# Optimization experiments

Measured on AMD Instinct MI355X. Metric: run time of the kernel, lower is better.

## Reference

```python
import jax, jax.numpy as jnp
import numpy as np

BATCH = 512
FEATURES = 256
BITS = 8
ENC = FEATURES * BITS          # 2048
HIDDEN = 8192
CLASSES = 1000
K_SYN = 32                     # synapses per segment
THRESH = 16                    # segmentActivationThreshold
VMIN, VMAX = 0.0, 1.0


def _make_synapse_matrix(key, num_neurons, prev_size, k):
    """Dense (num_neurons, prev_size) matrix with k random +/-1 synapses per neuron."""
    kc, ks = jax.random.split(key)
    cols = jax.random.randint(kc, (num_neurons, k), 0, prev_size)
    signs = jnp.where(jax.random.bernoulli(ks, 0.5, (num_neurons, k)), 1.0, -1.0)
    rows = jnp.broadcast_to(jnp.arange(num_neurons)[:, None], (num_neurons, k))
    W = jnp.zeros((num_neurons, prev_size), dtype=jnp.float32)
    return W.at[rows, cols].set(signs.astype(jnp.float32))


def gray_code_encode(x, num_bits, vmin, vmax):
    # (batch, features) -> (batch, features*bits) binary float
    levels = jnp.round(
        jnp.clip(x, vmin, vmax) / (vmax - vmin) * (2 ** num_bits - 1)
    ).astype(jnp.int32)
    gray = levels ^ (levels >> 1)
    bits = (gray[..., None] >> jnp.arange(num_bits)) & 1  # (b, f, bits)
    return bits.astype(jnp.float32).reshape(x.shape[0], -1)


def setup_inputs() -> dict:
    key = jax.random.key(0)
    kx, k1, k2, ko = jax.random.split(key, 4)
    x = jax.random.uniform(kx, (BATCH, FEATURES), dtype=jnp.float32)
    W1 = _make_synapse_matrix(k1, HIDDEN, ENC, K_SYN)
    W2 = _make_synapse_matrix(k2, HIDDEN, HIDDEN, K_SYN)
    # Output connections: float (useBinaryOutputConnections=False); small random
    # stand-in for trained connection strengths.
    Wout = jax.random.normal(ko, (2, HIDDEN, CLASSES), dtype=jnp.float32) * 0.02
    return {"x": x, "W1": W1, "W2": W2, "Wout": Wout}


def reference(x, W1, W2, Wout):
    # Encode continuous input to binary gray-code activations.
    a0 = gray_code_encode(x, BITS, VMIN, VMAX)          # (B, ENC)
    # Hidden layer 1: binary synapse matmul + threshold activation.
    z1 = a0 @ W1.T                                      # (B, HIDDEN)
    a1 = (z1 >= THRESH).astype(jnp.float32)
    # Hidden layer 2.
    z2 = a1 @ W2.T                                      # (B, HIDDEN)
    a2 = (z2 >= THRESH).astype(jnp.float32)
    # Output accumulation across all hidden layers.
    out = a1 @ Wout[0] + a2 @ Wout[1]                   # (B, CLASSES)
    predictions = jnp.argmax(out, axis=-1)
    return predictions, out
```

## Files before the change

kernel.cpp:

```cpp
#include <hip/hip_runtime.h>

#define BATCH 512
#define FEATURES 256
#define ENC 2048
#define HIDDEN 8192
#define CLASSES 1000
#define THRESH 16
#define MAXACT 256
#define NPREP 16
#define PAIR_CAP 65536

typedef unsigned long long u64;
typedef unsigned int u32;

#define OFF_A0T    0
#define OFF_NPAIRS 131072
#define OFF_PAIRS  131136


__global__ __launch_bounds__(256) void prep_kernel(const float* __restrict__ x,
                                                   u32* __restrict__ a0t_w,
                                                   u32* __restrict__ npairs) {
    int bid = blockIdx.x;
    int tid = threadIdx.x;
    if (bid == 0 && tid == 0) npairs[0] = 0;

    __shared__ float xs[32][256];
    for (int r = 0; r < 32; ++r)
        xs[r][tid] = x[(size_t)(bid * 32 + r) * FEATURES + tid];
    __syncthreads();

    u32 m[8] = {0,0,0,0,0,0,0,0};
    for (int i = 0; i < 32; ++i) {
        float v = xs[i][tid];
        v = fminf(fmaxf(v, 0.0f), 1.0f);
        int lvl = (int)rintf(v * 255.0f);
        int g = lvl ^ (lvl >> 1);
        u32 bit = 1u << i;
#pragma unroll
        for (int k = 0; k < 8; ++k) if ((g >> k) & 1) m[k] |= bit;
    }
#pragma unroll
    for (int k = 0; k < 8; ++k) a0t_w[(tid * 8 + k) * 16 + bid] = m[k];
}

__global__ __launch_bounds__(256) void z1_kernel(const float* __restrict__ W1,
                                                 const unsigned char* __restrict__ a0t,
                                                 u32* __restrict__ pairs,
                                                 u32* __restrict__ npairs) {
    int wid = threadIdx.x >> 6, lane = threadIdx.x & 63;
    int n = blockIdx.x * 4 + wid;
    const float4* rowv = reinterpret_cast<const float4*>(W1 + (size_t)n * ENC);
    __shared__ int colsAll[4][40];
    int* cols = colsAll[wid];

    float4 v[8];
#pragma unroll
    for (int it = 0; it < 8; ++it) v[it] = rowv[it * 64 + lane];

    int cnt = 0;
    u64 lmask = (lane == 63) ? 0x7fffffffffffffffULL : ((1ULL << lane) - 1ULL);
#pragma unroll
    for (int it = 0; it < 8; ++it) {
#pragma unroll
        for (int c = 0; c < 4; ++c) {
            float vc = (c == 0) ? v[it].x : (c == 1) ? v[it].y
                     : (c == 2) ? v[it].z : v[it].w;
            u64 mm = __ballot(vc != 0.0f);
            if (vc != 0.0f) {
                int pos = cnt + __popcll(mm & lmask);
                cols[pos] = ((it * 256 + lane * 4 + c) << 1) | (vc < 0.0f ? 1 : 0);
            }
            cnt += __popcll(mm);
        }
    }

    u32 p0=0,p1=0,p2=0,p3=0,p4=0,p5=0;
    u32 q0=0,q1=0,q2=0,q3=0,q4=0,q5=0;
#pragma unroll 8
    for (int i = 0; i < cnt; ++i) {
        int e = __builtin_amdgcn_readfirstlane(cols[i]);
        u32 m = a0t[(size_t)(e >> 1) * 64 + lane];
        if (e & 1) {
            u32 t;
            t = q0 & m; q0 ^= m; m = t;
            t = q1 & m; q1 ^= m; m = t;
            t = q2 & m; q2 ^= m; m = t;
            t = q3 & m; q3 ^= m; m = t;
            t = q4 & m; q4 ^= m; m = t;
            q5 ^= m;
        } else {
            u32 t;
            t = p0 & m; p0 ^= m; m = t;
            t = p1 & m; p1 ^= m; m = t;
            t = p2 & m; p2 ^= m; m = t;
            t = p3 & m; p3 ^= m; m = t;
            p5 ^= (p4 & m); p4 ^= m;
        }
    }

    u32 cand = p4 | p5;
    while (cand) {
        int k = __ffs(cand) - 1;
        cand &= cand - 1;
        int P = ((p0 >> k) & 1) | (((p1 >> k) & 1) << 1) | (((p2 >> k) & 1) << 2) |
                (((p3 >> k) & 1) << 3) | (((p4 >> k) & 1) << 4) | (((p5 >> k) & 1) << 5);
        int N = ((q0 >> k) & 1) | (((q1 >> k) & 1) << 1) | (((q2 >> k) & 1) << 2) |
                (((q3 >> k) & 1) << 3) | (((q4 >> k) & 1) << 4) | (((q5 >> k) & 1) << 5);
        if (P - N >= THRESH) {
            int b = lane * 8 + k;
            u32 pos = atomicAdd(npairs, 1u);
            if (pos < PAIR_CAP) pairs[pos] = ((u32)b << 13) | (u32)n;
        }
    }
}

__global__ __launch_bounds__(256) void out_kernel(const float* __restrict__ W2,
                                                  const float* __restrict__ Wout,
                                                  const u32* __restrict__ pairs,
                                                  const u32* __restrict__ npairs,
                                                  float* __restrict__ outp,
                                                  float* __restrict__ pred) {
    int b = blockIdx.x;
    int tid = threadIdx.x;
    __shared__ int act1[MAXACT], act2[MAXACT];
    __shared__ int n1s, n2s;
    __shared__ float rv[256];
    __shared__ int ri[256];

    if (tid == 0) { n1s = 0; n2s = 0; }
    __syncthreads();

    int tot = (int)npairs[0];
    if (tot > PAIR_CAP) tot = PAIR_CAP;
    for (int i = tid; i < tot; i += 256) {
        u32 p = pairs[i];
        if ((int)(p >> 13) == b) {
            int pos = atomicAdd(&n1s, 1);
            if (pos < MAXACT) act1[pos] = (int)(p & 8191u);
        }
    }
    __syncthreads();
    if (tid == 0) {
        int c = n1s; if (c > MAXACT) { c = MAXACT; n1s = c; }
        for (int i = 1; i < c; ++i) {
            int vv = act1[i], k = i;
            while (k > 0 && act1[k - 1] > vv) { act1[k] = act1[k - 1]; --k; }
            act1[k] = vv;
        }
    }
    __syncthreads();
    int na1 = n1s;

    if (na1 >= THRESH) {
        for (int nn = tid; nn < HIDDEN; nn += 256) {
            int z = 0;
            for (int i = 0; i < na1; ++i) z += (int)W2[(size_t)nn * HIDDEN + act1[i]];
            if (z >= THRESH) {
                int pos = atomicAdd(&n2s, 1);
                if (pos < MAXACT) act2[pos] = nn;
            }
        }
        __syncthreads();
        if (tid == 0) {
            int c = n2s; if (c > MAXACT) { c = MAXACT; n2s = c; }
            for (int i = 1; i < c; ++i) {
                int vv = act2[i], k = i;
                while (k > 0 && act2[k - 1] > vv) { act2[k] = act2[k - 1]; --k; }
                act2[k] = vv;
            }
        }
        __syncthreads();
    }
    int na2 = n2s;

    float s0 = 0.f, s1 = 0.f, s2 = 0.f, s3 = 0.f;
    for (int i = 0; i < na1; ++i) {
        const float* wr = Wout + (size_t)act1[i] * CLASSES;
        s0 += wr[tid]; s1 += wr[tid + 256]; s2 += wr[tid + 512];
        if (tid + 768 < CLASSES) s3 += wr[tid + 768];
    }
    for (int i = 0; i < na2; ++i) {
        const float* wr = Wout + (size_t)HIDDEN * CLASSES + (size_t)act2[i] * CLASSES;
        s0 += wr[tid]; s1 += wr[tid + 256]; s2 += wr[tid + 512];
        if (tid + 768 < CLASSES) s3 += wr[tid + 768];
    }

    float* orow = outp + (size_t)b * CLASSES;
    orow[tid] = s0; orow[tid + 256] = s1; orow[tid + 512] = s2;
    if (tid + 768 < CLASSES) orow[tid + 768] = s3;

    float best = s0; int bi = tid;
    if (s1 > best) { best = s1; bi = tid + 256; }
    if (s2 > best) { best = s2; bi = tid + 512; }
    if (tid + 768 < CLASSES && s3 > best) { best = s3; bi = tid + 768; }
    rv[tid] = best; ri[tid] = bi;
    __syncthreads();
    for (int off = 128; off; off >>= 1) {
        if (tid < off) {
            float ov = rv[tid + off]; int oi = ri[tid + off];
            if (ov > rv[tid] || (ov == rv[tid] && oi < ri[tid])) { rv[tid] = ov; ri[tid] = oi; }
        }
        __syncthreads();
    }
    if (tid == 0) pred[b] = (float)ri[0];
}

extern "C" void kernel_launch(void* const* d_in, const int* in_sizes, int n_in,
                              void* d_out, int out_size, void* d_ws, size_t ws_size,
                              hipStream_t stream) {
    (void)in_sizes; (void)n_in; (void)out_size; (void)ws_size;
    const float* x    = (const float*)d_in[0];
    const float* W1   = (const float*)d_in[1];
    const float* W2   = (const float*)d_in[2];
    const float* Wout = (const float*)d_in[3];

    float* pred = (float*)d_out;
    float* outp = (float*)d_out + BATCH;

    char* ws = (char*)d_ws;
    u32* a0t_w  = (u32*)(ws + OFF_A0T);
    u32* npairs = (u32*)(ws + OFF_NPAIRS);
    u32* pairs  = (u32*)(ws + OFF_PAIRS);

    prep_kernel<<<NPREP, 256, 0, stream>>>(x, a0t_w, npairs);
    z1_kernel<<<HIDDEN / 4, 256, 0, stream>>>(W1, (const unsigned char*)a0t_w,
                                              pairs, npairs);
    out_kernel<<<BATCH, 256, 0, stream>>>(W2, Wout, pairs, npairs, outp, pred);
}
```

Measured before the change: 38.20 us.

## Fuse gray-code prep into z1 kernel with per-block LDS bitmaps and slot output

Result: slower. 88.78 us (+132.4%).

```diff
diff --git a/kernel.cpp b/kernel.cpp
--- a/kernel.cpp
+++ b/kernel.cpp
@@ -7,118 +7,148 @@
 #define CLASSES 1000
 #define THRESH 16
 #define MAXACT 256
-#define NPREP 16
-#define PAIR_CAP 65536
+#define NBLK1 256
+#define THR1 1024
+#define ROWS_PER_BLK 32
+#define SLOTS 64
 
 typedef unsigned long long u64;
 typedef unsigned int u32;
 
-#define OFF_A0T    0
-#define OFF_NPAIRS 131072
-#define OFF_PAIRS  131136
-
-
-__global__ __launch_bounds__(256) void prep_kernel(const float* __restrict__ x,
-                                                   u32* __restrict__ a0t_w,
-                                                   u32* __restrict__ npairs) {
+#define OFF_CNTS  0
+#define OFF_PAIRS 1024
+
+__global__ __launch_bounds__(THR1, 4) void z1_fused(
+    const float* __restrict__ x, const float* __restrict__ W1,
+    u32* __restrict__ cnts, u32* __restrict__ pairs)
+{
+    __shared__ u32 a0t[ENC * 16];
+    __shared__ int colsAll[16][2][40];
+    __shared__ int lcnt;
+
+    int tid = threadIdx.x;
+    int wv = tid >> 6, lane = tid & 63;
     int bid = blockIdx.x;
-    int tid = threadIdx.x;
-    if (bid == 0 && tid == 0) npairs[0] = 0;
-
-    __shared__ float xs[32][256];
-    for (int r = 0; r < 32; ++r)
-        xs[r][tid] = x[(size_t)(bid * 32 + r) * FEATURES + tid];
-    __syncthreads();
-
-    u32 m[8] = {0,0,0,0,0,0,0,0};
-    for (int i = 0; i < 32; ++i) {
-        float v = xs[i][tid];
-        v = fminf(fmaxf(v, 0.0f), 1.0f);
-        int lvl = (int)rintf(v * 255.0f);
-        int g = lvl ^ (lvl >> 1);
-        u32 bit = 1u << i;
-#pragma unroll
-        for (int k = 0; k < 8; ++k) if ((g >> k) & 1) m[k] |= bit;
-    }
-#pragma unroll
-    for (int k = 0; k < 8; ++k) a0t_w[(tid * 8 + k) * 16 + bid] = m[k];
-}
-
-__global__ __launch_bounds__(256) void z1_kernel(const float* __restrict__ W1,
-                                                 const unsigned char* __restrict__ a0t,
-                                                 u32* __restrict__ pairs,
-                                                 u32* __restrict__ npairs) {
-    int wid = threadIdx.x >> 6, lane = threadIdx.x & 63;
-    int n = blockIdx.x * 4 + wid;
-    const float4* rowv = reinterpret_cast<const float4*>(W1 + (size_t)n * ENC);
-    __shared__ int colsAll[4][40];
-    int* cols = colsAll[wid];
-
-    float4 v[8];
-#pragma unroll
-    for (int it = 0; it < 8; ++it) v[it] = rowv[it * 64 + lane];
-
-    int cnt = 0;
+    if (tid == 0) lcnt = 0;
+
+    int n0 = bid * ROWS_PER_BLK + wv * 2;
+    const float4* r0 = reinterpret_cast<const float4*>(W1 + (size_t)n0 * ENC);
+    const float4* r1 = reinterpret_cast<const float4*>(W1 + (size_t)(n0 + 1) * ENC);
+    float4 va[8], vb[8];
+#pragma unroll
+    for (int it = 0; it < 8; ++it) va[it] = r0[it * 64 + lane];
+#pragma unroll
+    for (int it = 0; it < 8; ++it) vb[it] = r1[it * 64 + lane];
+
+    {
+        int w = tid & 15;
+        int fbase = tid >> 4;
+#pragma unroll
+        for (int j = 0; j < 4; ++j) {
+            int f = fbase + 64 * j;
+            u32 m[8] = {0, 0, 0, 0, 0, 0, 0, 0};
+#pragma unroll 4
+            for (int i = 0; i < 32; ++i) {
+                float v = x[(size_t)(w * 32 + i) * FEATURES + f];
+                v = fminf(fmaxf(v, 0.0f), 1.0f);
+                int lvl = (int)rintf(v * 255.0f);
+                int g = lvl ^ (lvl >> 1);
+#pragma unroll
+                for (int k = 0; k < 8; ++k)
+                    m[k] |= (u32)((g >> k) & 1) << i;
+            }
+#pragma unroll
+            for (int k = 0; k < 8; ++k)
+                a0t[(f * 8 + k) * 16 + w] = m[k];
+        }
+    }
+
     u64 lmask = (lane == 63) ? 0x7fffffffffffffffULL : ((1ULL << lane) - 1ULL);
+    int ca = 0, cb = 0;
 #pragma unroll
     for (int it = 0; it < 8; ++it) {
 #pragma unroll
         for (int c = 0; c < 4; ++c) {
-            float vc = (c == 0) ? v[it].x : (c == 1) ? v[it].y
-                     : (c == 2) ? v[it].z : v[it].w;
+            float vc = (c == 0) ? va[it].x : (c == 1) ? va[it].y
+                     : (c == 2) ? va[it].z : va[it].w;
             u64 mm = __ballot(vc != 0.0f);
             if (vc != 0.0f) {
-                int pos = cnt + __popcll(mm & lmask);
-                cols[pos] = ((it * 256 + lane * 4 + c) << 1) | (vc < 0.0f ? 1 : 0);
-            }
-            cnt += __popcll(mm);
-        }
-    }
-
-    u32 p0=0,p1=0,p2=0,p3=0,p4=0,p5=0;
-    u32 q0=0,q1=0,q2=0,q3=0,q4=0,q5=0;
+                int pos = ca + __popcll(mm & lmask);
+                colsAll[wv][0][pos] = ((it * 256 + lane * 4 + c) << 1) | (vc < 0.0f ? 1 : 0);
+            }
+            ca += __popcll(mm);
+        }
+    }
+#pragma unroll
+    for (int it = 0; it < 8; ++it) {
+#pragma unroll
+        for (int c = 0; c < 4; ++c) {
+            float vc = (c == 0) ? vb[it].x : (c == 1) ? vb[it].y
+                     : (c == 2) ? vb[it].z : vb[it].w;
+            u64 mm = __ballot(vc != 0.0f);
+            if (vc != 0.0f) {
+                int pos = cb + __popcll(mm & lmask);
+                colsAll[wv][1][pos] = ((it * 256 + lane * 4 + c) << 1) | (vc < 0.0f ? 1 : 0);
+            }
+            cb += __popcll(mm);
+        }
+    }
+
+    __syncthreads();
+
+    const unsigned char* a0b = (const unsigned char*)a0t;
+    for (int rr = 0; rr < 2; ++rr) {
+        int cnt = (rr == 0) ? ca : cb;
+        int n = n0 + rr;
+        const int* cols = colsAll[wv][rr];
+        u32 p0=0,p1=0,p2=0,p3=0,p4=0,p5=0;
+        u32 q0=0,q1=0,q2=0,q3=0,q4=0,q5=0;
 #pragma unroll 8
-    for (int i = 0; i < cnt; ++i) {
-        int e = __builtin_amdgcn_readfirstlane(cols[i]);
-        u32 m = a0t[(size_t)(e >> 1) * 64 + lane];
-        if (e & 1) {
-            u32 t;
-            t = q0 & m; q0 ^= m; m = t;
-            t = q1 & m; q1 ^= m; m = t;
-            t = q2 & m; q2 ^= m; m = t;
-            t = q3 & m; q3 ^= m; m = t;
-            t = q4 & m; q4 ^= m; m = t;
-            q5 ^= m;
-        } else {
-            u32 t;
-            t = p0 & m; p0 ^= m; m = t;
-            t = p1 & m; p1 ^= m; m = t;
-            t = p2 & m; p2 ^= m; m = t;
-            t = p3 & m; p3 ^= m; m = t;
-            p5 ^= (p4 & m); p4 ^= m;
-        }
-    }
-
-    u32 cand = p4 | p5;
-    while (cand) {
-        int k = __ffs(cand) - 1;
-        cand &= cand - 1;
-        int P = ((p0 >> k) & 1) | (((p1 >> k) & 1) << 1) | (((p2 >> k) & 1) << 2) |
-                (((p3 >> k) & 1) << 3) | (((p4 >> k) & 1) << 4) | (((p5 >> k) & 1) << 5);
-        int N = ((q0 >> k) & 1) | (((q1 >> k) & 1) << 1) | (((q2 >> k) & 1) << 2) |
-                (((q3 >> k) & 1) << 3) | (((q4 >> k) & 1) << 4) | (((q5 >> k) & 1) << 5);
-        if (P - N >= THRESH) {
-            int b = lane * 8 + k;
-            u32 pos = atomicAdd(npairs, 1u);
-            if (pos < PAIR_CAP) pairs[pos] = ((u32)b << 13) | (u32)n;
-        }
-    }
+        for (int i = 0; i < cnt; ++i) {
+            int e = __builtin_amdgcn_readfirstlane(cols[i]);
+            u32 m = a0b[(size_t)(e >> 1) * 64 + lane];
+            if (e & 1) {
+                u32 t;
+                t = q0 & m; q0 ^= m; m = t;
+                t = q1 & m; q1 ^= m; m = t;
+                t = q2 & m; q2 ^= m; m = t;
+                t = q3 & m; q3 ^= m; m = t;
+                t = q4 & m; q4 ^= m; m = t;
+                q5 ^= m;
+            } else {
+                u32 t;
+                t = p0 & m; p0 ^= m; m = t;
+                t = p1 & m; p1 ^= m; m = t;
+                t = p2 & m; p2 ^= m; m = t;
+                t = p3 & m; p3 ^= m; m = t;
+                p5 ^= (p4 & m); p4 ^= m;
+            }
+        }
+
+        u32 cand = p4 | p5;
+        while (cand) {
+            int k = __ffs(cand) - 1;
+            cand &= cand - 1;
+            int P = ((p0 >> k) & 1) | (((p1 >> k) & 1) << 1) | (((p2 >> k) & 1) << 2) |
+                    (((p3 >> k) & 1) << 3) | (((p4 >> k) & 1) << 4) | (((p5 >> k) & 1) << 5);
+            int N = ((q0 >> k) & 1) | (((q1 >> k) & 1) << 1) | (((q2 >> k) & 1) << 2) |
+                    (((q3 >> k) & 1) << 3) | (((q4 >> k) & 1) << 4) | (((q5 >> k) & 1) << 5);
+            if (P - N >= THRESH) {
+                int b = lane * 8 + k;
+                int pos = atomicAdd(&lcnt, 1);
+                if (pos < SLOTS) pairs[bid * SLOTS + pos] = ((u32)b << 13) | (u32)n;
+            }
+        }
+    }
+
+    __syncthreads();
+    if (tid == 0) { int c = lcnt; if (c > SLOTS) c = SLOTS; cnts[bid] = (u32)c; }
 }
 
 __global__ __launch_bounds__(256) void out_kernel(const float* __restrict__ W2,
                                                   const float* __restrict__ Wout,
                                                   const u32* __restrict__ pairs,
-                                                  const u32* __restrict__ npairs,
+                                                  const u32* __restrict__ cnts,
                                                   float* __restrict__ outp,
                                                   float* __restrict__ pred) {
     int b = blockIdx.x;
@@ -131,13 +161,15 @@
     if (tid == 0) { n1s = 0; n2s = 0; }
     __syncthreads();
 
-    int tot = (int)npairs[0];
-    if (tot > PAIR_CAP) tot = PAIR_CAP;
-    for (int i = tid; i < tot; i += 256) {
-        u32 p = pairs[i];
-        if ((int)(p >> 13) == b) {
-            int pos = atomicAdd(&n1s, 1);
-            if (pos < MAXACT) act1[pos] = (int)(p & 8191u);
+    for (int j = tid; j < NBLK1; j += 256) {
+        int c = (int)cnts[j];
+        if (c > SLOTS) c = SLOTS;
+        for (int i = 0; i < c; ++i) {
+            u32 p = pairs[j * SLOTS + i];
+            if ((int)(p >> 13) == b) {
+                int pos = atomicAdd(&n1s, 1);
+                if (pos < MAXACT) act1[pos] = (int)(p & 8191u);
+            }
         }
     }
     __syncthreads();
@@ -219,12 +251,9 @@
     float* outp = (float*)d_out + BATCH;
 
     char* ws = (char*)d_ws;
-    u32* a0t_w  = (u32*)(ws + OFF_A0T);
-    u32* npairs = (u32*)(ws + OFF_NPAIRS);
-    u32* pairs  = (u32*)(ws + OFF_PAIRS);
-
-    prep_kernel<<<NPREP, 256, 0, stream>>>(x, a0t_w, npairs);
-    z1_kernel<<<HIDDEN / 4, 256, 0, stream>>>(W1, (const unsigned char*)a0t_w,
-                                              pairs, npairs);
-    out_kernel<<<BATCH, 256, 0, stream>>>(W2, Wout, pairs, npairs, outp, pred);
+    u32* cnts  = (u32*)(ws + OFF_CNTS);
+    u32* pairs = (u32*)(ws + OFF_PAIRS);
+
+    z1_fused<<<NBLK1, THR1, 0, stream>>>(x, W1, cnts, pairs);
+    out_kernel<<<BATCH, 256, 0, stream>>>(W2, Wout, pairs, cnts, outp, pred);
 }
```
